# Kernel tuning notes

Measured on AMD Instinct MI355X. Metric: run time of the kernel, lower is better.

The kernel has to match this reference:

```python
import jax, jax.numpy as jnp
import numpy as np

B, Q, C = 2, 8192, 256
L, P, NH = 4, 4, 8
DH = C // NH
HMAX = 128  # max level resolution; smaller levels are zero-padded (mimics sparse COO extents)


def _inverse_sigmoid(x, eps=1e-5):
    x = jnp.clip(x, 0.0, 1.0)
    return jnp.log(jnp.clip(x, eps, None) / jnp.clip(1.0 - x, eps, None))


def setup_inputs() -> dict:
    key = jax.random.key(0)
    ks = jax.random.split(key, 8)
    query = jax.random.normal(ks[0], (Q, C), jnp.float32)
    xy_reference_points = jax.random.uniform(ks[1], (Q, 2), dtype=jnp.float32)
    spatial_shapes = jnp.array([[128, 128], [64, 64], [32, 32], [16, 16]], jnp.int32)
    values = jax.random.normal(ks[2], (B, HMAX, HMAX, L, C), jnp.float32)
    # zero out entries outside each level's (H_l, W_l) extent, like the sparse COO tensor
    ys = jnp.arange(HMAX)[:, None, None]
    xs = jnp.arange(HMAX)[None, :, None]
    mask = (ys < spatial_shapes[:, 0]) & (xs < spatial_shapes[:, 1])  # [HMAX, HMAX, L]
    values = values * mask[None, :, :, :, None]
    batch_offsets = jnp.array([0, Q // B], jnp.int32)
    s = 0.02
    W_so = jax.random.normal(ks[3], (L * P * NH * 2, C), jnp.float32) * s
    b_so = jax.random.normal(ks[4], (L * P * NH * 2,), jnp.float32) * 0.5
    W_aw = jax.random.normal(ks[5], (L * P * NH, C), jnp.float32) * s
    b_aw = jnp.zeros((L * P * NH,), jnp.float32)
    W_v = jax.random.normal(ks[6], (C, C), jnp.float32) * s
    b_v = jnp.zeros((C,), jnp.float32)
    W_o = jax.random.normal(ks[7], (C, C), jnp.float32) * s
    b_o = jnp.zeros((C,), jnp.float32)
    return dict(query=query, xy_reference_points=xy_reference_points, values=values,
                W_so=W_so, b_so=b_so, W_aw=W_aw, b_aw=b_aw, W_v=W_v, b_v=b_v,
                W_o=W_o, b_o=b_o, batch_offsets=batch_offsets, spatial_shapes=spatial_shapes)


def _forward(query, ref, values, W_so, b_so, W_aw, b_aw, W_v, b_v, W_o, b_o,
             batch_offsets, spatial_shapes):
    # value projection applied to (sparse) feature values, then split heads
    v = values @ W_v.T + b_v                      # [B, HMAX, HMAX, L, C]
    v = v.reshape(B, HMAX, HMAX, L, NH, DH)
    # sampling offsets and attention weights from queries
    offs = (query @ W_so.T + b_so).reshape(Q, L, P, NH, 2)
    aw = jax.nn.softmax((query @ W_aw.T + b_aw).reshape(Q, L * P, NH), axis=1)
    aw = aw.reshape(Q, L, P, NH)
    # sampling locations in (0,1), then grid_sample convention (align_corners=False)
    loc = jax.nn.sigmoid(_inverse_sigmoid(ref)[:, None, None, None, :] + offs)  # [Q,L,P,NH,2]
    g = loc * 2.0 - 1.0
    Hs = spatial_shapes[:, 0].astype(jnp.float32)[None, :, None, None]
    Ws = spatial_shapes[:, 1].astype(jnp.float32)[None, :, None, None]
    x = (g[..., 0] + 1.0) * Ws * 0.5 - 0.5        # [Q,L,P,NH] pixel coords
    y = (g[..., 1] + 1.0) * Hs * 0.5 - 0.5
    x0f = jnp.floor(x); y0f = jnp.floor(y)
    wx1 = x - x0f; wx0 = 1.0 - wx1
    wy1 = y - y0f; wy0 = 1.0 - wy1
    x0 = x0f.astype(jnp.int32); y0 = y0f.astype(jnp.int32)
    x1 = x0 + 1; y1 = y0 + 1
    # per-query batch index from batch_offsets
    b_idx = (jnp.searchsorted(batch_offsets, jnp.arange(Q), side='right') - 1)[:, None, None, None]
    l_idx = jnp.arange(L)[None, :, None, None]
    h_idx = jnp.arange(NH)[None, None, None, :]
    Hsi = spatial_shapes[:, 0][None, :, None, None]
    Wsi = spatial_shapes[:, 1][None, :, None, None]

    def corner(yi, xi):
        valid = (xi >= 0) & (xi < Wsi) & (yi >= 0) & (yi < Hsi)
        xc = jnp.clip(xi, 0, HMAX - 1)
        yc = jnp.clip(yi, 0, HMAX - 1)
        vals = v[b_idx, yc, xc, l_idx, h_idx]     # [Q, L, P, NH, DH]
        return vals * valid[..., None]

    sampled = (corner(y0, x0) * (wy0 * wx0)[..., None]
               + corner(y0, x1) * (wy0 * wx1)[..., None]
               + corner(y1, x0) * (wy1 * wx0)[..., None]
               + corner(y1, x1) * (wy1 * wx1)[..., None])  # [Q, L, P, NH, DH]
    out = jnp.einsum('qlphd,qlph->qhd', sampled, aw).reshape(Q, C)
    return out @ W_o.T + b_o


def reference(query, xy_reference_points, values, W_so, b_so, W_aw, b_aw,
              W_v, b_v, W_o, b_o, batch_offsets, spatial_shapes):
    return _forward(query, xy_reference_points, values, W_so, b_so, W_aw, b_aw,
                    W_v, b_v, W_o, b_o, batch_offsets, spatial_shapes)
```

## Files before the change

### kernel.cpp

```cpp
#include <hip/hip_runtime.h>
#include <math.h>

#define QTOT   8192
#define LNUM   4
#define PNUM   4
#define NHEAD  8
#define DHEAD  32
#define HMAX   128
#define NV_PER_B 21760
#define MROWS  (2 * NV_PER_B)
#define QPERB  4096

#define G1_MT  (MROWS / 128)
#define G1_BLKS (G1_MT * 2)
#define G2_BLKS (128 * 3)

typedef __attribute__((ext_vector_type(8))) short bf16x8;
typedef __attribute__((ext_vector_type(4))) float f32x4;

static __device__ __forceinline__ ushort bf16_hi(float f) {
    return (ushort)(__builtin_bit_cast(unsigned int, f) >> 16);
}
static __device__ __forceinline__ ushort bf16_lo(float f, ushort hi) {
    float hf = __builtin_bit_cast(float, ((unsigned int)hi) << 16);
    return (ushort)(__builtin_bit_cast(unsigned int, f - hf) >> 16);
}
static __device__ __forceinline__ ushort bf16_rne(float f) {
    unsigned u = __builtin_bit_cast(unsigned int, f);
    unsigned rr = (u + 0x7FFFu + ((u >> 16) & 1u)) >> 16;
    return (ushort)rr;
}

template<int GATHER, int BM, int NPROD, int OUTBF16>
__device__ __forceinline__
void gemm_body(const float* __restrict__ A,
               const float* __restrict__ B1,
               const float* __restrict__ B2,
               const float* __restrict__ bias1,
               const float* __restrict__ bias2,
               void* __restrict__ Out,
               int nsplit, int ldo, int bx, int by, char* smem)
{
    constexpr int MI  = BM / 32;
    constexpr int AIT = BM * 8 / 256;
    constexpr int PL  = (NPROD > 1) ? 2 : 1;
    ushort* sAp = (ushort*)smem;
    ushort* sBp = sAp + 2 * PL * BM * 32;
    int* rowBase = (int*)(sBp + 2 * PL * 128 * 32);

    const int tid = threadIdx.x;
    const int m0 = bx * BM;
    const int n0 = by * 128;

    if (GATHER) {
        for (int s = tid; s < BM; s += 256) {
            int r = m0 + s;
            int b = (r >= NV_PER_B) ? 1 : 0;
            int rp = r - b * NV_PER_B;
            int l, y, x;
            if (rp < 16384)      { l = 0; y = rp >> 7; x = rp & 127; }
            else if (rp < 20480) { int rr = rp - 16384; l = 1; y = rr >> 6; x = rr & 63; }
            else if (rp < 21504) { int rr = rp - 20480; l = 2; y = rr >> 5; x = rr & 31; }
            else                 { int rr = rp - 21504; l = 3; y = rr >> 4; x = rr & 15; }
            rowBase[s] = (((((b << 7) | y) << 7) | x) * 4 + l) << 8;
        }
        __syncthreads();
    }

    float4 pa[AIT], pb[4];

    auto loadA = [&](int kt) {
        #pragma unroll
        for (int i = 0; i < AIT; ++i) {
            int s = tid + i * 256;
            int r = s >> 3, c4 = s & 7;
            const float* src = GATHER
                ? A + rowBase[r] + kt * 32 + c4 * 4
                : A + (size_t)(m0 + r) * 256 + kt * 32 + c4 * 4;
            pa[i] = *(const float4*)src;
        }
        #pragma unroll
        for (int i = 0; i < 4; ++i) {
            int s = tid + i * 256;
            int r = s >> 3, c4 = s & 7;
            int bn = n0 + r;
            const float* src = ((bn < nsplit) ? B1 + (size_t)bn * 256
                                              : B2 + (size_t)(bn - nsplit) * 256)
                               + kt * 32 + c4 * 4;
            pb[i] = *(const float4*)src;
        }
    };

    auto writeLDS = [&](int buf) {
        #pragma unroll
        for (int i = 0; i < AIT; ++i) {
            int s = tid + i * 256;
            int r = s >> 3, c4 = s & 7;
            float4 v = pa[i];
            ushort4 hi;
            hi.x = bf16_hi(v.x); hi.y = bf16_hi(v.y);
            hi.z = bf16_hi(v.z); hi.w = bf16_hi(v.w);
            int idx = r * 32 + ((((c4 >> 1) ^ (r & 3)) << 3) | ((c4 & 1) << 2));
            *(ushort4*)&sAp[(buf * PL + 0) * BM * 32 + idx] = hi;
            if (NPROD > 1) {
                ushort4 lo;
                lo.x = bf16_lo(v.x, hi.x); lo.y = bf16_lo(v.y, hi.y);
                lo.z = bf16_lo(v.z, hi.z); lo.w = bf16_lo(v.w, hi.w);
                *(ushort4*)&sAp[(buf * PL + PL - 1) * BM * 32 + idx] = lo;
            }
        }
        #pragma unroll
        for (int i = 0; i < 4; ++i) {
            int s = tid + i * 256;
            int r = s >> 3, c4 = s & 7;
            float4 v = pb[i];
            ushort4 hi;
            hi.x = bf16_hi(v.x); hi.y = bf16_hi(v.y);
            hi.z = bf16_hi(v.z); hi.w = bf16_hi(v.w);
            int idx = r * 32 + ((((c4 >> 1) ^ (r & 3)) << 3) | ((c4 & 1) << 2));
            *(ushort4*)&sBp[(buf * PL + 0) * 128 * 32 + idx] = hi;
            if (NPROD > 1) {
                ushort4 lo;
                lo.x = bf16_lo(v.x, hi.x); lo.y = bf16_lo(v.y, hi.y);
                lo.z = bf16_lo(v.z, hi.z); lo.w = bf16_lo(v.w, hi.w);
                *(ushort4*)&sBp[(buf * PL + PL - 1) * 128 * 32 + idx] = lo;
            }
        }
    };

    const int lane = tid & 63;
    const int wid  = tid >> 6;
    const int wrow = (wid >> 1) * (BM / 2);
    const int wcol = (wid & 1) * 64;
    const int fr   = lane & 15;
    const int ks   = lane >> 4;

    f32x4 acc[MI][4] = {};

    loadA(0);
    writeLDS(0);

    for (int kt = 0; kt < 8; ++kt) {
        __syncthreads();
        if (kt < 7) loadA(kt + 1);

        const int buf = kt & 1;
        bf16x8 ah[MI], al[MI], bh[4], bl[4];
        #pragma unroll
        for (int mi = 0; mi < MI; ++mi) {
            int row = wrow + mi * 16 + fr;
            int idx = row * 32 + ((ks ^ (row & 3)) << 3);
            ah[mi] = *(const bf16x8*)&sAp[(buf * PL + 0) * BM * 32 + idx];
            if (NPROD > 1) al[mi] = *(const bf16x8*)&sAp[(buf * PL + PL - 1) * BM * 32 + idx];
        }
        #pragma unroll
        for (int ni = 0; ni < 4; ++ni) {
            int row = wcol + ni * 16 + fr;
            int idx = row * 32 + ((ks ^ (row & 3)) << 3);
            bh[ni] = *(const bf16x8*)&sBp[(buf * PL + 0) * 128 * 32 + idx];
            if (NPROD > 1) bl[ni] = *(const bf16x8*)&sBp[(buf * PL + PL - 1) * 128 * 32 + idx];
        }
        #pragma unroll
        for (int mi = 0; mi < MI; ++mi)
            #pragma unroll
            for (int ni = 0; ni < 4; ++ni) {
                acc[mi][ni] = __builtin_amdgcn_mfma_f32_16x16x32_bf16(ah[mi], bh[ni], acc[mi][ni], 0, 0, 0);
                if (NPROD > 1) {
                    acc[mi][ni] = __builtin_amdgcn_mfma_f32_16x16x32_bf16(ah[mi], bl[ni], acc[mi][ni], 0, 0, 0);
                    acc[mi][ni] = __builtin_amdgcn_mfma_f32_16x16x32_bf16(al[mi], bh[ni], acc[mi][ni], 0, 0, 0);
                }
            }

        if (kt < 7) writeLDS((kt + 1) & 1);
    }

    #pragma unroll
    for (int mi = 0; mi < MI; ++mi)
        #pragma unroll
        for (int ni = 0; ni < 4; ++ni) {
            int col = n0 + wcol + ni * 16 + fr;
            float bs = (col < nsplit) ? bias1[col] : bias2[col - nsplit];
            int rbase = m0 + wrow + mi * 16 + ks * 4;
            #pragma unroll
            for (int rr = 0; rr < 4; ++rr) {
                float val = acc[mi][ni][rr] + bs;
                if (OUTBF16)
                    ((ushort*)Out)[(size_t)(rbase + rr) * ldo + col] = bf16_rne(val);
                else
                    ((float*)Out)[(size_t)(rbase + rr) * ldo + col] = val;
            }
        }
}

__global__ __launch_bounds__(256)
void fused_g12(const float* __restrict__ values,
               const float* __restrict__ W_v,  const float* __restrict__ b_v,
               const float* __restrict__ query,
               const float* __restrict__ W_so, const float* __restrict__ W_aw,
               const float* __restrict__ b_so, const float* __restrict__ b_aw,
               ushort* __restrict__ vproj, float* __restrict__ qbuf)
{
    extern __shared__ char smem[];
    const int f = blockIdx.x;
    if (f < G1_BLKS) {
        gemm_body<1, 128, 1, 1>(values, W_v, W_v, b_v, b_v, vproj,
                                256, 256, f % G1_MT, f / G1_MT, smem);
    } else {
        const int g = f - G1_BLKS;
        gemm_body<0, 64, 3, 0>(query, W_so, W_aw, b_so, b_aw, qbuf,
                               256, 384, g % 128, g / 128, smem);
    }
}

__global__ __launch_bounds__(256)
void gemm_o(const float* __restrict__ mid,
            const float* __restrict__ W_o, const float* __restrict__ b_o,
            float* __restrict__ out)
{
    extern __shared__ char smem[];
    gemm_body<0, 64, 1, 0>(mid, W_o, W_o, b_o, b_o, out,
                           256, 256, blockIdx.x, blockIdx.y, smem);
}

__global__ __launch_bounds__(256)
void sample1(const ushort* __restrict__ vproj,
             const float* __restrict__ qbuf,
             const float* __restrict__ ref,
             float* __restrict__ mid)
{
    __shared__ int2  s_rw[128][4];
    __shared__ float s_logit[16][8];
    __shared__ float s_aw[16][8];

    const int tid = threadIdx.x;
    const int q = blockIdx.x;
    const int b = (q >= QPERB) ? 1 : 0;

    if (tid < 128) {
        const int c  = tid;
        const int lp = c >> 3;
        const int l  = lp >> 2;
        const float2 off = *(const float2*)&qbuf[(size_t)q * 384 + c * 2];
        float rx = fminf(fmaxf(ref[q * 2 + 0], 0.f), 1.f);
        float ry = fminf(fmaxf(ref[q * 2 + 1], 0.f), 1.f);
        const float eps = 1e-5f;
        const float isx = logf(fmaxf(rx, eps) / fmaxf(1.f - rx, eps));
        const float isy = logf(fmaxf(ry, eps) / fmaxf(1.f - ry, eps));
        const float locx = 1.f / (1.f + expf(-(isx + off.x)));
        const float locy = 1.f / (1.f + expf(-(isy + off.y)));
        const int Wl = HMAX >> l, Hl = HMAX >> l;
        const float x = locx * (float)Wl - 0.5f;
        const float y = locy * (float)Hl - 0.5f;
        const float x0f = floorf(x), y0f = floorf(y);
        const float wx1 = x - x0f, wx0 = 1.f - wx1;
        const float wy1 = y - y0f, wy0 = 1.f - wy1;
        const int x0 = (int)x0f, y0 = (int)y0f;
        const int lo = (l == 0) ? 0 : (l == 1) ? 16384 : (l == 2) ? 20480 : 21504;
        const int base = b * NV_PER_B + lo;
        const int   xs[2] = {x0, x0 + 1};
        const int   ys[2] = {y0, y0 + 1};
        const float wxs[2] = {wx0, wx1};
        const float wys[2] = {wy0, wy1};
        #pragma unroll
        for (int cy = 0; cy < 2; ++cy)
            #pragma unroll
            for (int cx = 0; cx < 2; ++cx) {
                const int xi = xs[cx], yi = ys[cy];
                const bool valid = (xi >= 0) & (xi < Wl) & (yi >= 0) & (yi < Hl);
                const int idx = cy * 2 + cx;
                s_rw[c][idx].x = valid ? (base + yi * Wl + xi) : 0;
                s_rw[c][idx].y = __float_as_int(valid ? (wys[cy] * wxs[cx]) : 0.f);
            }
        s_logit[lp][c & 7] = qbuf[(size_t)q * 384 + 256 + c];
    }
    __syncthreads();

    if (tid < 8) {
        const int h = tid;
        float m = -INFINITY;
        #pragma unroll
        for (int j = 0; j < 16; ++j) m = fmaxf(m, s_logit[j][h]);
        float s = 0.f;
        #pragma unroll
        for (int j = 0; j < 16; ++j) s += expf(s_logit[j][h] - m);
        const float inv = 1.f / s;
        #pragma unroll
        for (int j = 0; j < 16; ++j)
            s_aw[j][h] = expf(s_logit[j][h] - m) * inv;
    }
    __syncthreads();

    #pragma unroll
    for (int t2 = tid; t2 < 512; t2 += 256) {
        const int c = t2 >> 2, j = t2 & 3;
        const float aw = s_aw[c >> 3][c & 7];
        s_rw[c][j].y = __float_as_int(__int_as_float(s_rw[c][j].y) * aw);
    }
    __syncthreads();

    const int h  = tid >> 5;
    const int l5 = tid & 31;
    const int ds = l5 & 3;
    const int rt = l5 >> 2;
    const int j  = rt & 3;
    const int rtH = rt >> 2;

    float a0 = 0.f, a1 = 0.f, a2 = 0.f, a3 = 0.f;
    float a4 = 0.f, a5 = 0.f, a6 = 0.f, a7 = 0.f;
    #pragma unroll
    for (int it = 0; it < 8; ++it) {
        const int lp = 2 * it + rtH;
        const int c = lp * 8 + h;
        const int2 rw = s_rw[c][j];
        const float w = __int_as_float(rw.y);
        const uint4 u = *(const uint4*)&vproj[(size_t)rw.x * 256 + h * 32 + ds * 8];
        a0 = fmaf(w, __builtin_bit_cast(float, u.x << 16), a0);
        a1 = fmaf(w, __builtin_bit_cast(float, u.x & 0xFFFF0000u), a1);
        a2 = fmaf(w, __builtin_bit_cast(float, u.y << 16), a2);
        a3 = fmaf(w, __builtin_bit_cast(float, u.y & 0xFFFF0000u), a3);
        a4 = fmaf(w, __builtin_bit_cast(float, u.z << 16), a4);
        a5 = fmaf(w, __builtin_bit_cast(float, u.z & 0xFFFF0000u), a5);
        a6 = fmaf(w, __builtin_bit_cast(float, u.w << 16), a6);
        a7 = fmaf(w, __builtin_bit_cast(float, u.w & 0xFFFF0000u), a7);
    }
    #pragma unroll
    for (int m = 4; m <= 16; m <<= 1) {
        a0 += __shfl_xor(a0, m); a1 += __shfl_xor(a1, m);
        a2 += __shfl_xor(a2, m); a3 += __shfl_xor(a3, m);
        a4 += __shfl_xor(a4, m); a5 += __shfl_xor(a5, m);
        a6 += __shfl_xor(a6, m); a7 += __shfl_xor(a7, m);
    }
    if (rt == 0) {
        float* dst = &mid[(size_t)q * 256 + h * 32 + ds * 8];
        float4 o0 = {a0, a1, a2, a3};
        float4 o1 = {a4, a5, a6, a7};
        *(float4*)dst = o0;
        *(float4*)(dst + 4) = o1;
    }
}

extern "C" void kernel_launch(void* const* d_in, const int* in_sizes, int n_in,
                              void* d_out, int out_size, void* d_ws, size_t ws_size,
                              hipStream_t stream)
{
    const float* query  = (const float*)d_in[0];
    const float* ref    = (const float*)d_in[1];
    const float* values = (const float*)d_in[2];
    const float* W_so   = (const float*)d_in[3];
    const float* b_so   = (const float*)d_in[4];
    const float* W_aw   = (const float*)d_in[5];
    const float* b_aw   = (const float*)d_in[6];
    const float* W_v    = (const float*)d_in[7];
    const float* b_v    = (const float*)d_in[8];
    const float* W_o    = (const float*)d_in[9];
    const float* b_o    = (const float*)d_in[10];
    float* out = (float*)d_out;

    ushort* vproj = (ushort*)d_ws;
    float* qbuf  = (float*)d_ws + ((size_t)MROWS * 256 * 2) / 4;
    float* mid   = qbuf + (size_t)QTOT * 384;

    const int smem_bytes = 48 * 1024 + 1024;

    dim3 blk(256);
    fused_g12<<<dim3(G1_BLKS + G2_BLKS), blk, smem_bytes, stream>>>(
        values, W_v, b_v, query, W_so, W_aw, b_so, b_aw, vproj, qbuf);
    sample1<<<dim3(QTOT), blk, 0, stream>>>(vproj, qbuf, ref, mid);
    gemm_o<<<dim3(QTOT / 64, 2), blk, smem_bytes, stream>>>(mid, W_o, b_o, out);
}
```

Before: 266.6 us.

## Replace LDS-staged GEMM with direct global-to-register MFMA operand loads

The shared-memory double-buffered GEMM body is replaced by a version where each wave loads its A and B fragments straight from global memory into registers, converts them to bf16 and feeds MFMA without LDS or barriers. Tiles become 128x64 per block (32 rows per wave), and the grids for the fused value/query projection and the output projection are resized to match. This removes LDS traffic, swizzling and __syncthreads. In exchange, each wave reloads B rows from global/L2 with no sharing across waves, and global reads become strided per lane.

```diff
diff --git a/kernel.cpp b/kernel.cpp
--- a/kernel.cpp
+++ b/kernel.cpp
@@ -2,18 +2,13 @@
 #include <math.h>
 
 #define QTOT   8192
-#define LNUM   4
-#define PNUM   4
-#define NHEAD  8
-#define DHEAD  32
 #define HMAX   128
 #define NV_PER_B 21760
 #define MROWS  (2 * NV_PER_B)
 #define QPERB  4096
 
-#define G1_MT  (MROWS / 128)
-#define G1_BLKS (G1_MT * 2)
-#define G2_BLKS (128 * 3)
+#define G1_BLKS (340 * 4)
+#define G2_BLKS (64 * 6)
 
 typedef __attribute__((ext_vector_type(8))) short bf16x8;
 typedef __attribute__((ext_vector_type(4))) float f32x4;
@@ -30,160 +25,104 @@
     unsigned rr = (u + 0x7FFFu + ((u >> 16) & 1u)) >> 16;
     return (ushort)rr;
 }
-
-template<int GATHER, int BM, int NPROD, int OUTBF16>
+static __device__ __forceinline__ bf16x8 cvt_hi8(float4 v0, float4 v1) {
+    bf16x8 r;
+    r[0] = (short)bf16_hi(v0.x); r[1] = (short)bf16_hi(v0.y);
+    r[2] = (short)bf16_hi(v0.z); r[3] = (short)bf16_hi(v0.w);
+    r[4] = (short)bf16_hi(v1.x); r[5] = (short)bf16_hi(v1.y);
+    r[6] = (short)bf16_hi(v1.z); r[7] = (short)bf16_hi(v1.w);
+    return r;
+}
+static __device__ __forceinline__ bf16x8 cvt_lo8(float4 v0, float4 v1, bf16x8 h) {
+    bf16x8 r;
+    r[0] = (short)bf16_lo(v0.x, (ushort)h[0]); r[1] = (short)bf16_lo(v0.y, (ushort)h[1]);
+    r[2] = (short)bf16_lo(v0.z, (ushort)h[2]); r[3] = (short)bf16_lo(v0.w, (ushort)h[3]);
+    r[4] = (short)bf16_lo(v1.x, (ushort)h[4]); r[5] = (short)bf16_lo(v1.y, (ushort)h[5]);
+    r[6] = (short)bf16_lo(v1.z, (ushort)h[6]); r[7] = (short)bf16_lo(v1.w, (ushort)h[7]);
+    return r;
+}
+
+static __device__ __forceinline__ const float* gather_row_ptr(const float* A, int r) {
+    int b = (r >= NV_PER_B) ? 1 : 0;
+    int rp = r - b * NV_PER_B;
+    int l, y, x;
+    if (rp < 16384)      { l = 0; y = rp >> 7; x = rp & 127; }
+    else if (rp < 20480) { int rr = rp - 16384; l = 1; y = rr >> 6; x = rr & 63; }
+    else if (rp < 21504) { int rr = rp - 20480; l = 2; y = rr >> 5; x = rr & 31; }
+    else                 { int rr = rp - 21504; l = 3; y = rr >> 4; x = rr & 15; }
+    return A + ((size_t)((((((b << 7) | y) << 7) | x) * 4) + l) << 8);
+}
+
+template<int GATHER, int NPROD, int OUTBF16>
 __device__ __forceinline__
-void gemm_body(const float* __restrict__ A,
-               const float* __restrict__ B1,
-               const float* __restrict__ B2,
-               const float* __restrict__ bias1,
-               const float* __restrict__ bias2,
-               void* __restrict__ Out,
-               int nsplit, int ldo, int bx, int by, char* smem)
-{
-    constexpr int MI  = BM / 32;
-    constexpr int AIT = BM * 8 / 256;
-    constexpr int PL  = (NPROD > 1) ? 2 : 1;
-    ushort* sAp = (ushort*)smem;
-    ushort* sBp = sAp + 2 * PL * BM * 32;
-    int* rowBase = (int*)(sBp + 2 * PL * 128 * 32);
-
-    const int tid = threadIdx.x;
-    const int m0 = bx * BM;
-    const int n0 = by * 128;
-
-    if (GATHER) {
-        for (int s = tid; s < BM; s += 256) {
-            int r = m0 + s;
-            int b = (r >= NV_PER_B) ? 1 : 0;
-            int rp = r - b * NV_PER_B;
-            int l, y, x;
-            if (rp < 16384)      { l = 0; y = rp >> 7; x = rp & 127; }
-            else if (rp < 20480) { int rr = rp - 16384; l = 1; y = rr >> 6; x = rr & 63; }
-            else if (rp < 21504) { int rr = rp - 20480; l = 2; y = rr >> 5; x = rr & 31; }
-            else                 { int rr = rp - 21504; l = 3; y = rr >> 4; x = rr & 15; }
-            rowBase[s] = (((((b << 7) | y) << 7) | x) * 4 + l) << 8;
-        }
-        __syncthreads();
-    }
-
-    float4 pa[AIT], pb[4];
-
-    auto loadA = [&](int kt) {
-        #pragma unroll
-        for (int i = 0; i < AIT; ++i) {
-            int s = tid + i * 256;
-            int r = s >> 3, c4 = s & 7;
-            const float* src = GATHER
-                ? A + rowBase[r] + kt * 32 + c4 * 4
-                : A + (size_t)(m0 + r) * 256 + kt * 32 + c4 * 4;
-            pa[i] = *(const float4*)src;
-        }
-        #pragma unroll
-        for (int i = 0; i < 4; ++i) {
-            int s = tid + i * 256;
-            int r = s >> 3, c4 = s & 7;
-            int bn = n0 + r;
-            const float* src = ((bn < nsplit) ? B1 + (size_t)bn * 256
-                                              : B2 + (size_t)(bn - nsplit) * 256)
-                               + kt * 32 + c4 * 4;
-            pb[i] = *(const float4*)src;
-        }
-    };
-
-    auto writeLDS = [&](int buf) {
-        #pragma unroll
-        for (int i = 0; i < AIT; ++i) {
-            int s = tid + i * 256;
-            int r = s >> 3, c4 = s & 7;
-            float4 v = pa[i];
-            ushort4 hi;
-            hi.x = bf16_hi(v.x); hi.y = bf16_hi(v.y);
-            hi.z = bf16_hi(v.z); hi.w = bf16_hi(v.w);
-            int idx = r * 32 + ((((c4 >> 1) ^ (r & 3)) << 3) | ((c4 & 1) << 2));
-            *(ushort4*)&sAp[(buf * PL + 0) * BM * 32 + idx] = hi;
+void gemm_direct(const float* __restrict__ A,
+                 const float* __restrict__ B1,
+                 const float* __restrict__ B2,
+                 const float* __restrict__ bias1,
+                 const float* __restrict__ bias2,
+                 void* __restrict__ Out,
+                 int nsplit, int ldo, int bx, int by)
+{
+    const int tid  = threadIdx.x;
+    const int lane = tid & 63;
+    const int wid  = tid >> 6;
+    const int fr   = lane & 15;
+    const int ks   = lane >> 4;
+    const int m0   = bx * 128 + wid * 32;
+    const int n0   = by * 64;
+
+    const float* Arow0 = GATHER ? gather_row_ptr(A, m0 + fr)
+                                : A + (size_t)(m0 + fr) * 256;
+    const float* Arow1 = GATHER ? gather_row_ptr(A, m0 + 16 + fr)
+                                : A + (size_t)(m0 + 16 + fr) * 256;
+    const float* Brow[4];
+    #pragma unroll
+    for (int ni = 0; ni < 4; ++ni) {
+        const int col = n0 + ni * 16 + fr;
+        Brow[ni] = (col < nsplit) ? B1 + (size_t)col * 256
+                                  : B2 + (size_t)(col - nsplit) * 256;
+    }
+
+    f32x4 acc[2][4] = {};
+
+    #pragma unroll
+    for (int kt = 0; kt < 8; ++kt) {
+        const int ko = kt * 32 + ks * 8;
+        const float4 a00 = *(const float4*)(Arow0 + ko);
+        const float4 a01 = *(const float4*)(Arow0 + ko + 4);
+        const float4 a10 = *(const float4*)(Arow1 + ko);
+        const float4 a11 = *(const float4*)(Arow1 + ko + 4);
+        const bf16x8 ah0 = cvt_hi8(a00, a01);
+        const bf16x8 ah1 = cvt_hi8(a10, a11);
+        bf16x8 al0, al1;
+        if (NPROD > 1) { al0 = cvt_lo8(a00, a01, ah0); al1 = cvt_lo8(a10, a11, ah1); }
+        #pragma unroll
+        for (int ni = 0; ni < 4; ++ni) {
+            const float4 b0 = *(const float4*)(Brow[ni] + ko);
+            const float4 b1 = *(const float4*)(Brow[ni] + ko + 4);
+            const bf16x8 bh = cvt_hi8(b0, b1);
+            acc[0][ni] = __builtin_amdgcn_mfma_f32_16x16x32_bf16(ah0, bh, acc[0][ni], 0, 0, 0);
+            acc[1][ni] = __builtin_amdgcn_mfma_f32_16x16x32_bf16(ah1, bh, acc[1][ni], 0, 0, 0);
             if (NPROD > 1) {
-                ushort4 lo;
-                lo.x = bf16_lo(v.x, hi.x); lo.y = bf16_lo(v.y, hi.y);
-                lo.z = bf16_lo(v.z, hi.z); lo.w = bf16_lo(v.w, hi.w);
-                *(ushort4*)&sAp[(buf * PL + PL - 1) * BM * 32 + idx] = lo;
+                const bf16x8 bl = cvt_lo8(b0, b1, bh);
+                acc[0][ni] = __builtin_amdgcn_mfma_f32_16x16x32_bf16(ah0, bl, acc[0][ni], 0, 0, 0);
+                acc[0][ni] = __builtin_amdgcn_mfma_f32_16x16x32_bf16(al0, bh, acc[0][ni], 0, 0, 0);
+                acc[1][ni] = __builtin_amdgcn_mfma_f32_16x16x32_bf16(ah1, bl, acc[1][ni], 0, 0, 0);
+                acc[1][ni] = __builtin_amdgcn_mfma_f32_16x16x32_bf16(al1, bh, acc[1][ni], 0, 0, 0);
             }
         }
-        #pragma unroll
-        for (int i = 0; i < 4; ++i) {
-            int s = tid + i * 256;
-            int r = s >> 3, c4 = s & 7;
-            float4 v = pb[i];
-            ushort4 hi;
-            hi.x = bf16_hi(v.x); hi.y = bf16_hi(v.y);
-            hi.z = bf16_hi(v.z); hi.w = bf16_hi(v.w);
-            int idx = r * 32 + ((((c4 >> 1) ^ (r & 3)) << 3) | ((c4 & 1) << 2));
-            *(ushort4*)&sBp[(buf * PL + 0) * 128 * 32 + idx] = hi;
-            if (NPROD > 1) {
-                ushort4 lo;
-                lo.x = bf16_lo(v.x, hi.x); lo.y = bf16_lo(v.y, hi.y);
-                lo.z = bf16_lo(v.z, hi.z); lo.w = bf16_lo(v.w, hi.w);
-                *(ushort4*)&sBp[(buf * PL + PL - 1) * 128 * 32 + idx] = lo;
-            }
-        }
-    };
-
-    const int lane = tid & 63;
-    const int wid  = tid >> 6;
-    const int wrow = (wid >> 1) * (BM / 2);
-    const int wcol = (wid & 1) * 64;
-    const int fr   = lane & 15;
-    const int ks   = lane >> 4;
-
-    f32x4 acc[MI][4] = {};
-
-    loadA(0);
-    writeLDS(0);
-
-    for (int kt = 0; kt < 8; ++kt) {
-        __syncthreads();
-        if (kt < 7) loadA(kt + 1);
-
-        const int buf = kt & 1;
-        bf16x8 ah[MI], al[MI], bh[4], bl[4];
-        #pragma unroll
-        for (int mi = 0; mi < MI; ++mi) {
-            int row = wrow + mi * 16 + fr;
-            int idx = row * 32 + ((ks ^ (row & 3)) << 3);
-            ah[mi] = *(const bf16x8*)&sAp[(buf * PL + 0) * BM * 32 + idx];
-            if (NPROD > 1) al[mi] = *(const bf16x8*)&sAp[(buf * PL + PL - 1) * BM * 32 + idx];
-        }
+    }
+
+    #pragma unroll
+    for (int mi = 0; mi < 2; ++mi)
         #pragma unroll
         for (int ni = 0; ni < 4; ++ni) {
-            int row = wcol + ni * 16 + fr;
-            int idx = row * 32 + ((ks ^ (row & 3)) << 3);
-            bh[ni] = *(const bf16x8*)&sBp[(buf * PL + 0) * 128 * 32 + idx];
-            if (NPROD > 1) bl[ni] = *(const bf16x8*)&sBp[(buf * PL + PL - 1) * 128 * 32 + idx];
-        }
-        #pragma unroll
-        for (int mi = 0; mi < MI; ++mi)
-            #pragma unroll
-            for (int ni = 0; ni < 4; ++ni) {
-                acc[mi][ni] = __builtin_amdgcn_mfma_f32_16x16x32_bf16(ah[mi], bh[ni], acc[mi][ni], 0, 0, 0);
-                if (NPROD > 1) {
-                    acc[mi][ni] = __builtin_amdgcn_mfma_f32_16x16x32_bf16(ah[mi], bl[ni], acc[mi][ni], 0, 0, 0);
-                    acc[mi][ni] = __builtin_amdgcn_mfma_f32_16x16x32_bf16(al[mi], bh[ni], acc[mi][ni], 0, 0, 0);
-                }
-            }
-
-        if (kt < 7) writeLDS((kt + 1) & 1);
-    }
-
-    #pragma unroll
-    for (int mi = 0; mi < MI; ++mi)
-        #pragma unroll
-        for (int ni = 0; ni < 4; ++ni) {
-            int col = n0 + wcol + ni * 16 + fr;
-            float bs = (col < nsplit) ? bias1[col] : bias2[col - nsplit];
-            int rbase = m0 + wrow + mi * 16 + ks * 4;
+            const int col = n0 + ni * 16 + fr;
+            const float bs = (col < nsplit) ? bias1[col] : bias2[col - nsplit];
+            const int rbase = m0 + mi * 16 + ks * 4;
             #pragma unroll
             for (int rr = 0; rr < 4; ++rr) {
-                float val = acc[mi][ni][rr] + bs;
+                const float val = acc[mi][ni][rr] + bs;
                 if (OUTBF16)
                     ((ushort*)Out)[(size_t)(rbase + rr) * ldo + col] = bf16_rne(val);
                 else
@@ -200,15 +139,14 @@
                const float* __restrict__ b_so, const float* __restrict__ b_aw,
                ushort* __restrict__ vproj, float* __restrict__ qbuf)
 {
-    extern __shared__ char smem[];
     const int f = blockIdx.x;
     if (f < G1_BLKS) {
-        gemm_body<1, 128, 1, 1>(values, W_v, W_v, b_v, b_v, vproj,
-                                256, 256, f % G1_MT, f / G1_MT, smem);
+        gemm_direct<1, 1, 1>(values, W_v, W_v, b_v, b_v, vproj,
+                             256, 256, f % 340, f / 340);
     } else {
         const int g = f - G1_BLKS;
-        gemm_body<0, 64, 3, 0>(query, W_so, W_aw, b_so, b_aw, qbuf,
-                               256, 384, g % 128, g / 128, smem);
+        gemm_direct<0, 3, 0>(query, W_so, W_aw, b_so, b_aw, qbuf,
+                             256, 384, g % 64, g / 64);
     }
 }
 
@@ -217,9 +155,8 @@
             const float* __restrict__ W_o, const float* __restrict__ b_o,
             float* __restrict__ out)
 {
-    extern __shared__ char smem[];
-    gemm_body<0, 64, 1, 0>(mid, W_o, W_o, b_o, b_o, out,
-                           256, 256, blockIdx.x, blockIdx.y, smem);
+    gemm_direct<0, 1, 0>(mid, W_o, W_o, b_o, b_o, out,
+                         256, 256, blockIdx.x, blockIdx.y);
 }
 
 __global__ __launch_bounds__(256)
@@ -360,11 +297,9 @@
     float* qbuf  = (float*)d_ws + ((size_t)MROWS * 256 * 2) / 4;
     float* mid   = qbuf + (size_t)QTOT * 384;
 
-    const int smem_bytes = 48 * 1024 + 1024;
-
     dim3 blk(256);
-    fused_g12<<<dim3(G1_BLKS + G2_BLKS), blk, smem_bytes, stream>>>(
+    fused_g12<<<dim3(G1_BLKS + G2_BLKS), blk, 0, stream>>>(
         values, W_v, b_v, query, W_so, W_aw, b_so, b_aw, vproj, qbuf);
     sample1<<<dim3(QTOT), blk, 0, stream>>>(vproj, qbuf, ref, mid);
-    gemm_o<<<dim3(QTOT / 64, 2), blk, smem_bytes, stream>>>(mid, W_o, b_o, out);
-}
+    gemm_o<<<dim3(64, 4), blk, 0, stream>>>(mid, W_o, b_o, out);
+}
```

Result: slower. 317.1 us (+18.9%).
